# Kernel optimization log

Measured on AMD Instinct MI355X. Metric: run time of the kernel, lower is better.

The kernel has to match this reference:

```python
import jax, jax.numpy as jnp
import numpy as np

FEAT_DIM = 128
NODE_DIM = 64
BS, C, H, W = 32, 128, 64, 64
TOPK = 4096


def setup_inputs() -> dict:
    key = jax.random.key(0)
    k1, k2, k3, k4, k5, k6 = jax.random.split(key, 6)
    feature_map = jax.random.normal(k1, (BS, C, H, W), dtype=jnp.float32)
    # peak (row, col) coordinates in heatmap/feature space, floats in-range
    rc = jax.random.uniform(k2, (BS, TOPK, 2), dtype=jnp.float32)
    peak_coords = rc * jnp.array([H - 1, W - 1], dtype=jnp.float32)
    s1 = 1.0 / np.sqrt(FEAT_DIM)
    s2 = 1.0 / np.sqrt(NODE_DIM)
    W1 = jax.random.uniform(k3, (FEAT_DIM, NODE_DIM), jnp.float32, -s1, s1)
    b1 = jax.random.uniform(k4, (NODE_DIM,), jnp.float32, -s1, s1)
    W2 = jax.random.uniform(k5, (NODE_DIM, NODE_DIM), jnp.float32, -s2, s2)
    b2 = jax.random.uniform(k6, (NODE_DIM,), jnp.float32, -s2, s2)
    return {"feature_map": feature_map, "peak_coords": peak_coords,
            "W1": W1, "b1": b1, "W2": W2, "b2": b2}


def _bilinear_gather(feature_map, peak_coords):
    # feature_map: (bs, C, H, W); peak_coords: (bs, topk, 2) as (row, col)
    # Equivalent to F.grid_sample(mode='bilinear', align_corners=True) at
    # grid built from coords normalized by (H-1)/(W-1): the normalization
    # round-trips, so we sample directly at pixel coords (y, x).
    bs, c, h, w = feature_map.shape
    fm = jnp.transpose(feature_map, (0, 2, 3, 1))  # (bs, H, W, C)
    y = peak_coords[..., 0]
    x = peak_coords[..., 1]
    y0 = jnp.floor(y)
    x0 = jnp.floor(x)
    ty = y - y0
    tx = x - x0
    y0i = jnp.clip(y0.astype(jnp.int32), 0, h - 1)
    x0i = jnp.clip(x0.astype(jnp.int32), 0, w - 1)
    y1i = jnp.clip(y0i + 1, 0, h - 1)
    x1i = jnp.clip(x0i + 1, 0, w - 1)
    b = jnp.arange(bs, dtype=jnp.int32)[:, None]  # (bs, 1)
    v00 = fm[b, y0i, x0i]  # (bs, topk, C)
    v01 = fm[b, y0i, x1i]
    v10 = fm[b, y1i, x0i]
    v11 = fm[b, y1i, x1i]
    ty = ty[..., None]
    tx = tx[..., None]
    top = v00 * (1 - tx) + v01 * tx
    bot = v10 * (1 - tx) + v11 * tx
    return top * (1 - ty) + bot * ty  # (bs, topk, C)


def reference(feature_map, peak_coords, W1, b1, W2, b2):
    sampled = _bilinear_gather(feature_map, peak_coords)  # (bs, topk, C)
    h = jax.nn.relu(jnp.einsum('btc,cd->btd', sampled, W1) + b1)
    e = jnp.einsum('btd,de->bte', h, W2) + b2  # (bs, topk, node_dim)
    norm = jnp.linalg.norm(e, axis=-1, keepdims=True)
    return e / jnp.maximum(norm, 1e-12)
```

## Files before the change

### kernel.cpp

```cpp
#include <hip/hip_runtime.h>

#define Hh 64
#define Ww 64
#define Cc 128
#define ND 64
#define BSz 32
#define TOPK 4096
#define HW (Hh * Ww)
#define NPX (BSz * HW)

typedef short bf16x8 __attribute__((ext_vector_type(8)));
typedef unsigned short u16x8 __attribute__((ext_vector_type(8)));
typedef float f32x4 __attribute__((ext_vector_type(4)));

static __device__ __forceinline__ unsigned short f2bf(float f) {
    unsigned int u = __builtin_bit_cast(unsigned int, f);
    u += 0x7fffu + ((u >> 16) & 1u);
    return (unsigned short)(u >> 16);
}
static __device__ __forceinline__ float bf2f(unsigned short s) {
    unsigned int u = ((unsigned int)s) << 16;
    return __builtin_bit_cast(float, u);
}

__global__ __launch_bounds__(256) void k_mlp1(const float* __restrict__ fm,
                                              const float* __restrict__ W1,
                                              unsigned short* __restrict__ U) {
    __shared__ __align__(16) unsigned short w1s[8192];
    const int t = threadIdx.x;
#pragma unroll
    for (int k = 0; k < 32; ++k) {
        int i = t + 256 * k;
        int j = i & 7, l = (i >> 3) & 63, kk = (i >> 9) & 3, nt = i >> 11;
        int c = kk * 32 + 8 * (l >> 4) + j, n = nt * 16 + (l & 15);
        w1s[i] = f2bf(W1[c * ND + n]);
    }
    __syncthreads();

    const int bid = blockIdx.x;
    const int swz = (bid & 7) * 128 + (bid >> 3);
    const int lane = t & 63, wv = t >> 6;
    const int g = lane >> 4, mr = lane & 15;
    const int p0  = swz * 128 + wv * 32;
    const int b   = p0 >> 12;
    const int pin = p0 & 4095;
    const float* fb = fm + (size_t)b * (Cc * HW);

    bf16x8 aF[2][4];
#pragma unroll
    for (int half = 0; half < 2; ++half) {
        const int px = pin + half * 16 + mr;
#pragma unroll
        for (int kk = 0; kk < 4; ++kk) {
            float v[8];
#pragma unroll
            for (int j = 0; j < 8; ++j)
                v[j] = fb[(size_t)(kk * 32 + 8 * g + j) * HW + px];
            u16x8 o;
#pragma unroll
            for (int j = 0; j < 8; ++j) o[j] = f2bf(v[j]);
            aF[half][kk] = __builtin_bit_cast(bf16x8, o);
        }
    }

    f32x4 acc[2][4];
#pragma unroll
    for (int mt = 0; mt < 2; ++mt)
#pragma unroll
        for (int nt = 0; nt < 4; ++nt) acc[mt][nt] = (f32x4){0.f, 0.f, 0.f, 0.f};

#pragma unroll
    for (int kk = 0; kk < 4; ++kk)
#pragma unroll
        for (int nt = 0; nt < 4; ++nt) {
            bf16x8 bF = *(const bf16x8*)&w1s[((nt * 4 + kk) * 64 + lane) * 8];
            acc[0][nt] = __builtin_amdgcn_mfma_f32_16x16x32_bf16(aF[0][kk], bF, acc[0][nt], 0, 0, 0);
            acc[1][nt] = __builtin_amdgcn_mfma_f32_16x16x32_bf16(aF[1][kk], bF, acc[1][nt], 0, 0, 0);
        }

#pragma unroll
    for (int mt = 0; mt < 2; ++mt)
#pragma unroll
        for (int nt = 0; nt < 4; ++nt)
#pragma unroll
            for (int r = 0; r < 4; ++r) {
                const int row = p0 + mt * 16 + 4 * g + r;
                U[(size_t)row * ND + nt * 16 + mr] = f2bf(acc[mt][nt][r]);
            }
}

__global__ __launch_bounds__(256) void k_fused2(const unsigned short* __restrict__ U,
                                                const float* __restrict__ pc,
                                                const float* __restrict__ W2,
                                                const float* __restrict__ b1,
                                                const float* __restrict__ b2,
                                                float* __restrict__ out) {
    __shared__ __align__(16) unsigned short w2s[4096];
    __shared__ __align__(16) float b1s[64];
    __shared__ __align__(16) float b2s[64];
    const int t = threadIdx.x;
#pragma unroll
    for (int k = 0; k < 16; ++k) {
        int i = t + 256 * k;
        int j = i & 7, l = (i >> 3) & 63, kk = (i >> 9) & 1, nt = (i >> 10) & 3;
        int c = kk * 32 + 8 * (l >> 4) + j, n = nt * 16 + (l & 15);
        w2s[i] = f2bf(W2[c * ND + n]);
    }
    if (t < 64) { b1s[t] = b1[t]; b2s[t] = b2[t]; }
    __syncthreads();

    const int bid = blockIdx.x;
    const int swz = (bid & 7) * 256 + (bid >> 3);
    const int lane = t & 63, wv = t >> 6;
    const int g = lane >> 4, mr = lane & 15;
    const int m0 = swz * 64 + wv * 16;
    const int sm = m0 + mr;

    const float y = pc[2 * (size_t)sm + 0];
    const float x = pc[2 * (size_t)sm + 1];
    const float yf = floorf(y), xf = floorf(x);
    const float ty = y - yf, tx = x - xf;
    int y0 = min(max((int)yf, 0), Hh - 1);
    int x0 = min(max((int)xf, 0), Ww - 1);
    int y1 = min(y0 + 1, Hh - 1);
    int x1 = min(x0 + 1, Ww - 1);
    const float w00 = (1.f - ty) * (1.f - tx), w01 = (1.f - ty) * tx;
    const float w10 = ty * (1.f - tx),         w11 = ty * tx;
    const int bb = sm >> 12;
    const unsigned short* Ub = U + (size_t)bb * (HW * ND) + 8 * g;
    const u16x8* q00 = (const u16x8*)(Ub + (y0 * Ww + x0) * ND);
    const u16x8* q01 = (const u16x8*)(Ub + (y0 * Ww + x1) * ND);
    const u16x8* q10 = (const u16x8*)(Ub + (y1 * Ww + x0) * ND);
    const u16x8* q11 = (const u16x8*)(Ub + (y1 * Ww + x1) * ND);

    u16x8 r00[2], r01[2], r10[2], r11[2];
#pragma unroll
    for (int kk = 0; kk < 2; ++kk) {
        r00[kk] = q00[kk * 4];
        r01[kk] = q01[kk * 4];
        r10[kk] = q10[kk * 4];
        r11[kk] = q11[kk * 4];
    }

    bf16x8 aF[2];
#pragma unroll
    for (int kk = 0; kk < 2; ++kk) {
        f32x4 bA = *(const f32x4*)&b1s[kk * 32 + 8 * g];
        f32x4 bB = *(const f32x4*)&b1s[kk * 32 + 8 * g + 4];
        u16x8 o;
#pragma unroll
        for (int j = 0; j < 8; ++j) {
            float v = w00 * bf2f(r00[kk][j]) + w01 * bf2f(r01[kk][j])
                    + w10 * bf2f(r10[kk][j]) + w11 * bf2f(r11[kk][j]);
            float bv = (j < 4) ? bA[j & 3] : bB[j & 3];
            o[j] = f2bf(fmaxf(v + bv, 0.f));
        }
        aF[kk] = __builtin_bit_cast(bf16x8, o);
    }

    f32x4 acc2[4];
#pragma unroll
    for (int nt = 0; nt < 4; ++nt) {
        const float bc = b2s[nt * 16 + mr];
        acc2[nt] = (f32x4){bc, bc, bc, bc};
    }
#pragma unroll
    for (int kk = 0; kk < 2; ++kk)
#pragma unroll
        for (int nt = 0; nt < 4; ++nt) {
            bf16x8 bF = *(const bf16x8*)&w2s[((nt * 2 + kk) * 64 + lane) * 8];
            acc2[nt] = __builtin_amdgcn_mfma_f32_16x16x32_bf16(aF[kk], bF, acc2[nt], 0, 0, 0);
        }

    f32x4 ss = (f32x4){0.f, 0.f, 0.f, 0.f};
#pragma unroll
    for (int nt = 0; nt < 4; ++nt)
#pragma unroll
        for (int r = 0; r < 4; ++r) ss[r] += acc2[nt][r] * acc2[nt][r];
#pragma unroll
    for (int off = 1; off <= 8; off <<= 1) {
#pragma unroll
        for (int r = 0; r < 4; ++r) ss[r] += __shfl_xor(ss[r], off);
    }
#pragma unroll
    for (int r = 0; r < 4; ++r) {
        const float inv = 1.f / fmaxf(sqrtf(ss[r]), 1e-12f);
        const size_t ob = (size_t)(m0 + 4 * g + r) * ND;
#pragma unroll
        for (int nt = 0; nt < 4; ++nt)
            out[ob + nt * 16 + mr] = acc2[nt][r] * inv;
    }
}

extern "C" void kernel_launch(void* const* d_in, const int* in_sizes, int n_in,
                              void* d_out, int out_size, void* d_ws, size_t ws_size,
                              hipStream_t stream) {
    const float* fm = (const float*)d_in[0];
    const float* pc = (const float*)d_in[1];
    const float* W1 = (const float*)d_in[2];
    const float* b1 = (const float*)d_in[3];
    const float* W2 = (const float*)d_in[4];
    const float* b2 = (const float*)d_in[5];
    float* out = (float*)d_out;

    unsigned short* U = (unsigned short*)d_ws;

    k_mlp1<<<NPX / 128, 256, 0, stream>>>(fm, W1, U);
    k_fused2<<<(BSz * TOPK) / 64, 256, 0, stream>>>(U, pc, W2, b1, b2, out);
}
```

Measured before the change: 42.68 us.

## Process two row tiles per wave in fused kernel and coalesce weight staging loads

The second kernel now gives each wave two 16-row tiles instead of one and halves the grid, so the W2/bias staging into shared memory is amortized over twice as many points and each loaded W2 fragment feeds two MFMAs. Both kernels also read W1/W2 contiguously from global memory and scatter the values into the swizzled shared layout, rather than gathering strided global reads. This raises register use and lowers block count, which may reduce occupancy and latency hiding for the random bilinear gathers.

Result: faster. 36.21 us (-15.2%).

```diff
diff --git a/kernel.cpp b/kernel.cpp
--- a/kernel.cpp
+++ b/kernel.cpp
@@ -31,9 +31,10 @@
 #pragma unroll
     for (int k = 0; k < 32; ++k) {
         int i = t + 256 * k;
-        int j = i & 7, l = (i >> 3) & 63, kk = (i >> 9) & 3, nt = i >> 11;
-        int c = kk * 32 + 8 * (l >> 4) + j, n = nt * 16 + (l & 15);
-        w1s[i] = f2bf(W1[c * ND + n]);
+        int c = i >> 6, n = i & 63;
+        int kk = c >> 5, gg = (c >> 3) & 3, j = c & 7;
+        int nt = n >> 4, mr2 = n & 15;
+        w1s[((nt * 4 + kk) * 64 + gg * 16 + mr2) * 8 + j] = f2bf(W1[i]);
     }
     __syncthreads();
 
@@ -102,93 +103,106 @@
 #pragma unroll
     for (int k = 0; k < 16; ++k) {
         int i = t + 256 * k;
-        int j = i & 7, l = (i >> 3) & 63, kk = (i >> 9) & 1, nt = (i >> 10) & 3;
-        int c = kk * 32 + 8 * (l >> 4) + j, n = nt * 16 + (l & 15);
-        w2s[i] = f2bf(W2[c * ND + n]);
+        int c = i >> 6, n = i & 63;
+        int kk = c >> 5, gg = (c >> 3) & 3, j = c & 7;
+        int nt = n >> 4, mr2 = n & 15;
+        w2s[((nt * 2 + kk) * 64 + gg * 16 + mr2) * 8 + j] = f2bf(W2[i]);
     }
     if (t < 64) { b1s[t] = b1[t]; b2s[t] = b2[t]; }
     __syncthreads();
 
     const int bid = blockIdx.x;
-    const int swz = (bid & 7) * 256 + (bid >> 3);
+    const int swz = (bid & 7) * 128 + (bid >> 3);
     const int lane = t & 63, wv = t >> 6;
     const int g = lane >> 4, mr = lane & 15;
-    const int m0 = swz * 64 + wv * 16;
-    const int sm = m0 + mr;
-
-    const float y = pc[2 * (size_t)sm + 0];
-    const float x = pc[2 * (size_t)sm + 1];
-    const float yf = floorf(y), xf = floorf(x);
-    const float ty = y - yf, tx = x - xf;
-    int y0 = min(max((int)yf, 0), Hh - 1);
-    int x0 = min(max((int)xf, 0), Ww - 1);
-    int y1 = min(y0 + 1, Hh - 1);
-    int x1 = min(x0 + 1, Ww - 1);
-    const float w00 = (1.f - ty) * (1.f - tx), w01 = (1.f - ty) * tx;
-    const float w10 = ty * (1.f - tx),         w11 = ty * tx;
-    const int bb = sm >> 12;
+    const int m0 = swz * 128 + wv * 32;
+    const int bb = m0 >> 12;
     const unsigned short* Ub = U + (size_t)bb * (HW * ND) + 8 * g;
-    const u16x8* q00 = (const u16x8*)(Ub + (y0 * Ww + x0) * ND);
-    const u16x8* q01 = (const u16x8*)(Ub + (y0 * Ww + x1) * ND);
-    const u16x8* q10 = (const u16x8*)(Ub + (y1 * Ww + x0) * ND);
-    const u16x8* q11 = (const u16x8*)(Ub + (y1 * Ww + x1) * ND);
-
-    u16x8 r00[2], r01[2], r10[2], r11[2];
-#pragma unroll
-    for (int kk = 0; kk < 2; ++kk) {
-        r00[kk] = q00[kk * 4];
-        r01[kk] = q01[kk * 4];
-        r10[kk] = q10[kk * 4];
-        r11[kk] = q11[kk * 4];
-    }
-
-    bf16x8 aF[2];
-#pragma unroll
-    for (int kk = 0; kk < 2; ++kk) {
-        f32x4 bA = *(const f32x4*)&b1s[kk * 32 + 8 * g];
-        f32x4 bB = *(const f32x4*)&b1s[kk * 32 + 8 * g + 4];
-        u16x8 o;
-#pragma unroll
-        for (int j = 0; j < 8; ++j) {
-            float v = w00 * bf2f(r00[kk][j]) + w01 * bf2f(r01[kk][j])
-                    + w10 * bf2f(r10[kk][j]) + w11 * bf2f(r11[kk][j]);
-            float bv = (j < 4) ? bA[j & 3] : bB[j & 3];
-            o[j] = f2bf(fmaxf(v + bv, 0.f));
-        }
-        aF[kk] = __builtin_bit_cast(bf16x8, o);
-    }
-
-    f32x4 acc2[4];
-#pragma unroll
-    for (int nt = 0; nt < 4; ++nt) {
-        const float bc = b2s[nt * 16 + mr];
-        acc2[nt] = (f32x4){bc, bc, bc, bc};
-    }
+
+    float w00[2], w01[2], w10[2], w11[2];
+    const u16x8* q[2][4];
+#pragma unroll
+    for (int h = 0; h < 2; ++h) {
+        const int sm = m0 + h * 16 + mr;
+        const float y = pc[2 * (size_t)sm + 0];
+        const float x = pc[2 * (size_t)sm + 1];
+        const float yf = floorf(y), xf = floorf(x);
+        const float ty = y - yf, tx = x - xf;
+        int y0 = min(max((int)yf, 0), Hh - 1);
+        int x0 = min(max((int)xf, 0), Ww - 1);
+        int y1 = min(y0 + 1, Hh - 1);
+        int x1 = min(x0 + 1, Ww - 1);
+        w00[h] = (1.f - ty) * (1.f - tx); w01[h] = (1.f - ty) * tx;
+        w10[h] = ty * (1.f - tx);         w11[h] = ty * tx;
+        q[h][0] = (const u16x8*)(Ub + (y0 * Ww + x0) * ND);
+        q[h][1] = (const u16x8*)(Ub + (y0 * Ww + x1) * ND);
+        q[h][2] = (const u16x8*)(Ub + (y1 * Ww + x0) * ND);
+        q[h][3] = (const u16x8*)(Ub + (y1 * Ww + x1) * ND);
+    }
+    u16x8 rg[2][8];
+#pragma unroll
+    for (int h = 0; h < 2; ++h)
+#pragma unroll
+        for (int c2 = 0; c2 < 4; ++c2) {
+            rg[h][c2 * 2 + 0] = q[h][c2][0];
+            rg[h][c2 * 2 + 1] = q[h][c2][4];
+        }
+
+    bf16x8 aF[2][2];
+#pragma unroll
+    for (int h = 0; h < 2; ++h)
+#pragma unroll
+        for (int kk = 0; kk < 2; ++kk) {
+            f32x4 bA = *(const f32x4*)&b1s[kk * 32 + 8 * g];
+            f32x4 bB = *(const f32x4*)&b1s[kk * 32 + 8 * g + 4];
+            u16x8 o;
+#pragma unroll
+            for (int j = 0; j < 8; ++j) {
+                float v = w00[h] * bf2f(rg[h][0 + kk][j]) + w01[h] * bf2f(rg[h][2 + kk][j])
+                        + w10[h] * bf2f(rg[h][4 + kk][j]) + w11[h] * bf2f(rg[h][6 + kk][j]);
+                float bv = (j < 4) ? bA[j & 3] : bB[j & 3];
+                o[j] = f2bf(fmaxf(v + bv, 0.f));
+            }
+            aF[h][kk] = __builtin_bit_cast(bf16x8, o);
+        }
+
+    f32x4 acc2[2][4];
+#pragma unroll
+    for (int mt = 0; mt < 2; ++mt)
+#pragma unroll
+        for (int nt = 0; nt < 4; ++nt) {
+            const float bc = b2s[nt * 16 + mr];
+            acc2[mt][nt] = (f32x4){bc, bc, bc, bc};
+        }
 #pragma unroll
     for (int kk = 0; kk < 2; ++kk)
 #pragma unroll
         for (int nt = 0; nt < 4; ++nt) {
             bf16x8 bF = *(const bf16x8*)&w2s[((nt * 2 + kk) * 64 + lane) * 8];
-            acc2[nt] = __builtin_amdgcn_mfma_f32_16x16x32_bf16(aF[kk], bF, acc2[nt], 0, 0, 0);
-        }
-
-    f32x4 ss = (f32x4){0.f, 0.f, 0.f, 0.f};
-#pragma unroll
-    for (int nt = 0; nt < 4; ++nt)
-#pragma unroll
-        for (int r = 0; r < 4; ++r) ss[r] += acc2[nt][r] * acc2[nt][r];
-#pragma unroll
-    for (int off = 1; off <= 8; off <<= 1) {
-#pragma unroll
-        for (int r = 0; r < 4; ++r) ss[r] += __shfl_xor(ss[r], off);
-    }
-#pragma unroll
-    for (int r = 0; r < 4; ++r) {
-        const float inv = 1.f / fmaxf(sqrtf(ss[r]), 1e-12f);
-        const size_t ob = (size_t)(m0 + 4 * g + r) * ND;
+            acc2[0][nt] = __builtin_amdgcn_mfma_f32_16x16x32_bf16(aF[0][kk], bF, acc2[0][nt], 0, 0, 0);
+            acc2[1][nt] = __builtin_amdgcn_mfma_f32_16x16x32_bf16(aF[1][kk], bF, acc2[1][nt], 0, 0, 0);
+        }
+
+#pragma unroll
+    for (int mt = 0; mt < 2; ++mt) {
+        f32x4 ss = (f32x4){0.f, 0.f, 0.f, 0.f};
 #pragma unroll
         for (int nt = 0; nt < 4; ++nt)
-            out[ob + nt * 16 + mr] = acc2[nt][r] * inv;
+#pragma unroll
+            for (int r = 0; r < 4; ++r) ss[r] += acc2[mt][nt][r] * acc2[mt][nt][r];
+#pragma unroll
+        for (int off = 1; off <= 8; off <<= 1) {
+#pragma unroll
+            for (int r = 0; r < 4; ++r) ss[r] += __shfl_xor(ss[r], off);
+        }
+#pragma unroll
+        for (int r = 0; r < 4; ++r) {
+            const float inv = 1.f / fmaxf(sqrtf(ss[r]), 1e-12f);
+            const size_t ob = (size_t)(m0 + mt * 16 + 4 * g + r) * ND;
+#pragma unroll
+            for (int nt = 0; nt < 4; ++nt)
+                out[ob + nt * 16 + mr] = acc2[mt][nt][r] * inv;
+        }
     }
 }
 
@@ -206,5 +220,5 @@
     unsigned short* U = (unsigned short*)d_ws;
 
     k_mlp1<<<NPX / 128, 256, 0, stream>>>(fm, W1, U);
-    k_fused2<<<(BSz * TOPK) / 64, 256, 0, stream>>>(U, pc, W2, b1, b2, out);
-}
+    k_fused2<<<NPX / 128, 256, 0, stream>>>(U, pc, W2, b1, b2, out);
+}
```
